# Kernel optimization log

Measured on AMD Instinct MI355X. Metric: run time of the kernel, lower is better.

## Reference

```python
import jax, jax.numpy as jnp
import numpy as np

S_DIM = 128            # attention head width s
E_DIM = 1024           # expansion e = 2*hidden
SQRT_S = 128.0 ** 0.5
EPS = 1e-5


def setup_inputs() -> dict:
    key = jax.random.key(0)
    ks = jax.random.split(key, 8)
    B, S, H = 64, 512, 512
    uv_dim = 2 * E_DIM + S_DIM  # 2176
    # xavier-uniform-ish scale for uv weight
    lim = (6.0 / (H + uv_dim)) ** 0.5
    return {
        "x": jax.random.normal(ks[0], (B, S, H), dtype=jnp.float32),
        "ln_g": jnp.ones((1,), dtype=jnp.float32),
        "uv_w": jax.random.uniform(ks[1], (uv_dim, H), minval=-lim, maxval=lim, dtype=jnp.float32),
        "uv_b": jnp.zeros((uv_dim,), dtype=jnp.float32),
        "gamma": jax.random.uniform(ks[2], (2, S_DIM), dtype=jnp.float32),
        "beta": jax.random.uniform(ks[3], (2, S_DIM), dtype=jnp.float32),
        "w_bias": jax.random.uniform(ks[4], (2 * S - 1,), dtype=jnp.float32),
        "o_w": jax.random.normal(ks[5], (H, E_DIM), dtype=jnp.float32) * 0.02,
        "o_b": jnp.zeros((H,), dtype=jnp.float32),
    }


def _rope(x):
    # x: [B, S, 2, s]; rotate along the sequence dim (dim=1)
    S = x.shape[1]
    half = x.shape[-1] // 2
    pos = jnp.arange(S, dtype=jnp.float32)
    # torch: freq_seq = -arange(half)/half; inv_freq = 10000**(-freq_seq)
    inv_freq = 10000.0 ** (jnp.arange(half, dtype=jnp.float32) / half)
    sinus = pos[:, None, None] * inv_freq[None, None, :]  # [S, 1, half]
    sin, cos = jnp.sin(sinus), jnp.cos(sinus)
    x1, x2 = x[..., :half], x[..., half:]
    return jnp.concatenate([x1 * cos - x2 * sin, x2 * cos + x1 * sin], axis=-1)


def reference(x, ln_g, uv_w, uv_b, gamma, beta, w_bias, o_w, o_b):
    B, S, H = x.shape
    # ScaleNorm
    norm = jnp.linalg.norm(x, axis=-1, keepdims=True) * (H ** -0.5)
    xn = x / jnp.maximum(norm, EPS) * ln_g
    # fused uv projection + SiLU
    act = jax.nn.silu(xn @ uv_w.T + uv_b)  # [B, S, 2e+s]
    u = act[..., :E_DIM]
    v = act[..., E_DIM:2 * E_DIM]
    base = act[..., 2 * E_DIM:]                      # [B, S, s]
    base = base[:, :, None, :] * gamma + beta        # [B, S, 2, s]
    base = _rope(base)
    q, k = base[:, :, 0, :], base[:, :, 1, :]
    # scores + relative position bias: bias[i, j] = w[j - i + S - 1]
    qk = jnp.einsum('bsd,btd->bst', q, k)
    idx = jnp.arange(S)[None, :] - jnp.arange(S)[:, None] + (S - 1)
    qk = qk + w_bias[idx]
    # relu2 similarity kernel
    kernel = jnp.square(jax.nn.relu(qk / SQRT_S))    # [B, S, S]
    out = u * jnp.einsum('bst,bte->bse', kernel, v)  # gated attention
    out = out @ o_w.T + o_b
    return out + x  # use_shortcut: hidden == output
```

## Files before the change

### kernel.cpp

```cpp
#include <hip/hip_runtime.h>
#include <math.h>


#define M_TOT   32768
#define S_LEN   512
#define H_DIM   512
#define E_DIMC  1024
#define UV_DIM  2176
#define UV_PAD  2304
#define D_DIM   128

using floatx4  = __attribute__((ext_vector_type(4))) float;
using uintx2   = __attribute__((ext_vector_type(2))) unsigned int;
using uintx4   = __attribute__((ext_vector_type(4))) unsigned int;
using ushortx4 = __attribute__((ext_vector_type(4))) unsigned short;
using short8   = __attribute__((ext_vector_type(8))) short;

#define ASYNC_CP16(gsrc, ldst)                                                  \
    __builtin_amdgcn_global_load_lds(                                           \
        (const __attribute__((address_space(1))) void*)(gsrc),                  \
        (__attribute__((address_space(3))) void*)(ldst), 16, 0, 0)

__device__ __forceinline__ float bf2f(unsigned short h) {
    union { unsigned int u; float f; } c;
    c.u = ((unsigned int)h) << 16;
    return c.f;
}
__device__ __forceinline__ unsigned short f2bf(float f) {
    union { float f; unsigned int u; } c;
    c.f = f;
    unsigned int r = c.u + 0x7fffu + ((c.u >> 16) & 1u);
    return (unsigned short)(r >> 16);
}
__device__ __forceinline__ float silu_fast(float x) {
    float e = __expf(-x);
    return x * __builtin_amdgcn_rcpf(1.0f + e);
}
__device__ __forceinline__ int xcd_remap(int b, int nwg) {
    return (b & 7) * (nwg >> 3) + (b >> 3);
}

__global__ __launch_bounds__(256) void f2bf_kernel(const float* __restrict__ in,
                                                   unsigned short* __restrict__ out,
                                                   int n4) {
    int i = blockIdx.x * 256 + threadIdx.x;
    if (i < n4) {
        floatx4 v = ((const floatx4*)in)[i];
        ushortx4 o;
        o.x = f2bf(v.x); o.y = f2bf(v.y); o.z = f2bf(v.z); o.w = f2bf(v.w);
        ((ushortx4*)out)[i] = o;
    }
}

__global__ __launch_bounds__(256) void f2bf_pad_kernel(const float* __restrict__ in,
                                                       unsigned short* __restrict__ out,
                                                       int n4_src, int n4_dst) {
    int i = blockIdx.x * 256 + threadIdx.x;
    if (i < n4_dst) {
        ushortx4 o;
        if (i < n4_src) {
            floatx4 v = ((const floatx4*)in)[i];
            o.x = f2bf(v.x); o.y = f2bf(v.y); o.z = f2bf(v.z); o.w = f2bf(v.w);
        } else {
            o.x = 0; o.y = 0; o.z = 0; o.w = 0;
        }
        ((ushortx4*)out)[i] = o;
    }
}

__global__ __launch_bounds__(256) void rmsnorm_kernel(const float* __restrict__ x,
                                                      const float* __restrict__ ln_g,
                                                      unsigned short* __restrict__ xn) {
    int row  = blockIdx.x * 4 + (threadIdx.x >> 6);
    int lane = threadIdx.x & 63;
    const float* xr = x + (size_t)row * H_DIM;
    floatx4 v0 = ((const floatx4*)xr)[lane];
    floatx4 v1 = ((const floatx4*)xr)[lane + 64];
    float ss = v0.x*v0.x + v0.y*v0.y + v0.z*v0.z + v0.w*v0.w
             + v1.x*v1.x + v1.y*v1.y + v1.z*v1.z + v1.w*v1.w;
    #pragma unroll
    for (int off = 32; off > 0; off >>= 1) ss += __shfl_xor(ss, off, 64);
    float norm = sqrtf(ss) * 0.044194173824159216f;
    float sc   = ln_g[0] / fmaxf(norm, 1e-5f);
    unsigned short* xo = xn + (size_t)row * H_DIM;
    ushortx4 o0, o1;
    o0.x = f2bf(v0.x * sc); o0.y = f2bf(v0.y * sc);
    o0.z = f2bf(v0.z * sc); o0.w = f2bf(v0.w * sc);
    o1.x = f2bf(v1.x * sc); o1.y = f2bf(v1.y * sc);
    o1.z = f2bf(v1.z * sc); o1.w = f2bf(v1.w * sc);
    ((ushortx4*)xo)[lane]      = o0;
    ((ushortx4*)xo)[lane + 64] = o1;
}

__global__ __launch_bounds__(64) void rope_table_kernel(float* __restrict__ cost,
                                                        float* __restrict__ sint) {
    int s = blockIdx.x;
    int j = threadIdx.x;
    float invf = (float)pow(10000.0, (double)j / 64.0);
    float ang  = (float)s * invf;
    double a   = (double)ang;
    cost[s * 64 + j] = (float)cos(a);
    sint[s * 64 + j] = (float)sin(a);
}

__global__ __launch_bounds__(256) void rope_apply_kernel(const float* __restrict__ base,
                                                         const float* __restrict__ gamma,
                                                         const float* __restrict__ beta,
                                                         const float* __restrict__ cost,
                                                         const float* __restrict__ sint,
                                                         unsigned short* __restrict__ q,
                                                         unsigned short* __restrict__ k) {
    int idx = blockIdx.x * 256 + threadIdx.x;
    int m = idx >> 6;
    int j = idx & 63;
    int s = m & (S_LEN - 1);
    float b1 = base[(size_t)m * D_DIM + j];
    float b2 = base[(size_t)m * D_DIM + 64 + j];
    float c  = cost[s * 64 + j];
    float sn = sint[s * 64 + j];
    float yq1 = b1 * gamma[j]       + beta[j];
    float yq2 = b2 * gamma[64 + j]  + beta[64 + j];
    float yk1 = b1 * gamma[128 + j] + beta[128 + j];
    float yk2 = b2 * gamma[192 + j] + beta[192 + j];
    q[(size_t)m * D_DIM + j]      = f2bf(yq1 * c - yq2 * sn);
    q[(size_t)m * D_DIM + 64 + j] = f2bf(yq2 * c + yq1 * sn);
    k[(size_t)m * D_DIM + j]      = f2bf(yk1 * c - yk2 * sn);
    k[(size_t)m * D_DIM + 64 + j] = f2bf(yk2 * c + yk1 * sn);
}

template <bool SWAPT>
__device__ __forceinline__ void gemm256_core(const unsigned short* __restrict__ A,
                                             const unsigned short* __restrict__ B,
                                             int lda, int ldb, int K,
                                             int m0, int n0,
                                             unsigned short (&st)[4][2][128][64],
                                             floatx4 (&acc)[8][4]) {
    const int tid  = threadIdx.x;
    const int lane = tid & 63;
    const int wave = tid >> 6;
    const int quad = lane >> 4;
    const int l16  = lane & 15;
    const int wrow = (wave >> 2) * 128;
    const int wcol = (wave & 3) * 64;

    const int q0    = wave * 128 + lane;
    const int R0    = q0 >> 3;
    const int cp0   = q0 & 7;
    const int c0    = cp0 ^ (R0 & 7);
    const int srow0 = 2 * R0 + (c0 >> 2);
    const int scol0 = (c0 & 3) * 8;

    const unsigned short* pa0 = A + (size_t)(m0 + srow0) * lda + scol0;
    const unsigned short* pa1 = pa0 + (size_t)16 * lda;
    const unsigned short* pb0 = B + (size_t)(n0 + srow0) * ldb + scol0;
    const unsigned short* pb1 = pb0 + (size_t)16 * ldb;
    const int ldsOff0 = (wave * 128) * 8;
    const int ldsOff1 = (wave * 128 + 64) * 8;

    #pragma unroll
    for (int i = 0; i < 8; i++)
        #pragma unroll
        for (int j = 0; j < 4; j++) acc[i][j] = (floatx4){0.f, 0.f, 0.f, 0.f};

    const int NT = K >> 5;
    auto stage = [&](int t) {
        unsigned short* sA = &st[t & 3][0][0][0];
        unsigned short* sB = &st[t & 3][1][0][0];
        const int kt = t * 32;
        ASYNC_CP16(pa0 + kt, sA + ldsOff0);
        ASYNC_CP16(pa1 + kt, sA + ldsOff1);
        ASYNC_CP16(pb0 + kt, sB + ldsOff0);
        ASYNC_CP16(pb1 + kt, sB + ldsOff1);
    };
    stage(0);
    stage(1);
    stage(2);

    int aoff[8], boff[4];
    #pragma unroll
    for (int mt = 0; mt < 8; mt++) {
        int r  = wrow + mt * 16 + l16;
        int Rr = r >> 1;
        int cp = (((r & 1) << 2) + quad) ^ (Rr & 7);
        aoff[mt] = Rr * 64 + cp * 8;
    }
    #pragma unroll
    for (int nt = 0; nt < 4; nt++) {
        int r  = wcol + nt * 16 + l16;
        int Rr = r >> 1;
        int cp = (((r & 1) << 2) + quad) ^ (Rr & 7);
        boff[nt] = Rr * 64 + cp * 8;
    }

    for (int t = 0; t < NT; ++t) {
        if (t < NT - 2)       asm volatile("s_waitcnt vmcnt(8)" ::: "memory");
        else if (t == NT - 2) asm volatile("s_waitcnt vmcnt(4)" ::: "memory");
        else                  asm volatile("s_waitcnt vmcnt(0)" ::: "memory");
        __builtin_amdgcn_sched_barrier(0);
        __builtin_amdgcn_s_barrier();
        __builtin_amdgcn_sched_barrier(0);
        if (t + 3 < NT) stage(t + 3);

        const unsigned short* sA = &st[t & 3][0][0][0];
        const unsigned short* sB = &st[t & 3][1][0][0];
        short8 bf[4];
        #pragma unroll
        for (int nt = 0; nt < 4; nt++) {
            union { short8 s8; uintx4 u4; } fu;
            fu.u4 = *(const uintx4*)&sB[boff[nt]];
            bf[nt] = fu.s8;
        }
        #pragma unroll
        for (int half = 0; half < 2; half++) {
            short8 af[4];
            #pragma unroll
            for (int mt = 0; mt < 4; mt++) {
                union { short8 s8; uintx4 u4; } fu;
                fu.u4 = *(const uintx4*)&sA[aoff[half * 4 + mt]];
                af[mt] = fu.s8;
            }
            __builtin_amdgcn_s_setprio(1);
            #pragma unroll
            for (int mt = 0; mt < 4; mt++)
                #pragma unroll
                for (int nt = 0; nt < 4; nt++)
                    acc[half * 4 + mt][nt] = SWAPT
                        ? __builtin_amdgcn_mfma_f32_16x16x32_bf16(bf[nt], af[mt], acc[half * 4 + mt][nt], 0, 0, 0)
                        : __builtin_amdgcn_mfma_f32_16x16x32_bf16(af[mt], bf[nt], acc[half * 4 + mt][nt], 0, 0, 0);
            __builtin_amdgcn_s_setprio(0);
        }
    }
}

union __align__(16) Lds256 {
    unsigned short st[4][2][128][64];
    unsigned short T[256 * 256];
};

__global__ __launch_bounds__(512, 2) void gemm1_256_kernel(const unsigned short* __restrict__ xn,
                                                           const unsigned short* __restrict__ uvw,
                                                           const float* __restrict__ uvb,
                                                           unsigned short* __restrict__ u,
                                                           unsigned short* __restrict__ vT,
                                                           float* __restrict__ base) {
    __shared__ Lds256 lds;
    floatx4 acc[8][4];
    const int bl = blockIdx.y * 9 + blockIdx.x;
    const int lg = xcd_remap(bl, 9 * (M_TOT / 256));
    const int xb = lg % 9;
    const int m0 = (lg / 9) * 256;
    const int tid = threadIdx.x, lane = tid & 63, wave = tid >> 6;
    const int quad = lane >> 4, l16 = lane & 15;
    const int wrow = (wave >> 2) * 128, wcol = (wave & 3) * 64;

    if (xb < 4) {
        const int n0 = xb * 256;
        gemm256_core<true>(xn, uvw, H_DIM, H_DIM, H_DIM, m0, n0, lds.st, acc);
        __syncthreads();
        #pragma unroll
        for (int mt = 0; mt < 8; mt++) {
            int row = wrow + mt * 16 + l16;
            #pragma unroll
            for (int nt = 0; nt < 4; nt++) {
                int nl = wcol + nt * 16 + quad * 4;
                floatx4 b4 = *(const floatx4*)&uvb[n0 + nl];
                ushortx4 pk;
                #pragma unroll
                for (int r = 0; r < 4; r++)
                    pk[r] = f2bf(silu_fast(acc[mt][nt][r] + b4[r]));
                *(uintx2*)&lds.T[row * 256 + (((nl >> 3) ^ (row & 15)) & 31) * 8 + (nl & 7)] = *(uintx2*)&pk;
            }
        }
        __syncthreads();
        #pragma unroll
        for (int i = 0; i < 16; i++) {
            int idx = tid + i * 512;
            int row = idx >> 5, c16 = idx & 31;
            *(uintx4*)(u + (size_t)(m0 + row) * E_DIMC + n0 + c16 * 8) =
                *(const uintx4*)&lds.T[row * 256 + ((c16 ^ (row & 15)) * 8)];
        }
    } else if (xb < 8) {
        const int n0 = xb * 256;
        gemm256_core<false>(xn, uvw, H_DIM, H_DIM, H_DIM, m0, n0, lds.st, acc);
        __syncthreads();
        #pragma unroll
        for (int nt = 0; nt < 4; nt++) {
            int rowT = wcol + nt * 16 + l16;
            float bias = uvb[n0 + rowT];
            #pragma unroll
            for (int mt = 0; mt < 8; mt++) {
                int colT = wrow + mt * 16 + quad * 4;
                ushortx4 pk;
                #pragma unroll
                for (int r = 0; r < 4; r++)
                    pk[r] = f2bf(silu_fast(acc[mt][nt][r] + bias));
                *(uintx2*)&lds.T[rowT * 256 + (((colT >> 3) ^ (rowT & 15)) & 31) * 8 + (colT & 7)] = *(uintx2*)&pk;
            }
        }
        __syncthreads();
        const int b = m0 >> 9, sg0 = m0 & (S_LEN - 1), eg0 = n0 - E_DIMC;
        #pragma unroll
        for (int i = 0; i < 16; i++) {
            int idx = tid + i * 512;
            int e = idx >> 5, c16 = idx & 31;
            *(uintx4*)(vT + ((size_t)b * E_DIMC + eg0 + e) * S_LEN + sg0 + c16 * 8) =
                *(const uintx4*)&lds.T[e * 256 + ((c16 ^ (e & 15)) * 8)];
        }
    } else {
        const int n0 = 2048;
        gemm256_core<false>(xn, uvw, H_DIM, H_DIM, H_DIM, m0, n0, lds.st, acc);
        if ((wave & 3) < 2) {
            #pragma unroll
            for (int mt = 0; mt < 8; mt++) {
                int m = m0 + wrow + mt * 16 + quad * 4;
                #pragma unroll
                for (int nt = 0; nt < 4; nt++) {
                    int n = wcol + nt * 16 + l16;
                    float bias = uvb[2048 + n];
                    #pragma unroll
                    for (int r = 0; r < 4; r++)
                        base[(size_t)(m + r) * D_DIM + n] = silu_fast(acc[mt][nt][r] + bias);
                }
            }
        }
    }
}

__global__ __launch_bounds__(512, 2) void gemm_out256_kernel(const unsigned short* __restrict__ oe,
                                                             const unsigned short* __restrict__ ow,
                                                             const float* __restrict__ ob,
                                                             const float* __restrict__ x,
                                                             float* __restrict__ out) {
    __shared__ __align__(16) unsigned short st[4][2][128][64];
    floatx4 acc[8][4];
    const int bl = blockIdx.y * 2 + blockIdx.x;
    const int lg = xcd_remap(bl, 2 * (M_TOT / 256));
    const int n0 = (lg & 1) * 256;
    const int m0 = (lg >> 1) * 256;
    gemm256_core<true>(oe, ow, E_DIMC, E_DIMC, E_DIMC, m0, n0, st, acc);

    const int tid = threadIdx.x, lane = tid & 63, wave = tid >> 6;
    const int quad = lane >> 4, l16 = lane & 15;
    const int wrow = (wave >> 2) * 128, wcol = (wave & 3) * 64;
    #pragma unroll
    for (int mt = 0; mt < 8; mt++) {
        int m = m0 + wrow + mt * 16 + l16;
        #pragma unroll
        for (int nt = 0; nt < 4; nt++) {
            int n = n0 + wcol + nt * 16 + quad * 4;
            size_t off = (size_t)m * H_DIM + n;
            floatx4 b4 = *(const floatx4*)&ob[n];
            floatx4 x4 = *(const floatx4*)&x[off];
            *(floatx4*)&out[off] = acc[mt][nt] + b4 + x4;
        }
    }
}

struct GemmLds {
    unsigned short As[128 * 64];
    unsigned short Bs[128 * 64];
};

template <bool SWAPT>
__device__ __forceinline__ void gemm_bt_core(const unsigned short* __restrict__ A,
                                             const unsigned short* __restrict__ B,
                                             int lda, int ldb, int K,
                                             int m0, int n0,
                                             GemmLds& lds, floatx4 (&acc)[4][4]) {
    const int tid  = threadIdx.x;
    const int lane = tid & 63;
    const int wave = tid >> 6;
    const int quad = lane >> 4;
    const int l16  = lane & 15;
    const int wm   = (wave >> 1) * 64;
    const int wn   = (wave & 1) * 64;
    const int lrow = lane >> 3;
    const int cgs  = ((lane & 7) ^ lrow) * 8;

    #pragma unroll
    for (int i = 0; i < 4; i++)
        #pragma unroll
        for (int j = 0; j < 4; j++) acc[i][j] = (floatx4){0.f, 0.f, 0.f, 0.f};

    for (int kt = 0; kt < K; kt += 64) {
        #pragma unroll
        for (int i = 0; i < 4; i++) {
            int r0 = wave * 32 + i * 8;
            const unsigned short* ga = A + (size_t)(m0 + r0 + lrow) * lda + kt + cgs;
            const unsigned short* gb = B + (size_t)(n0 + r0 + lrow) * ldb + kt + cgs;
            ASYNC_CP16(ga, &lds.As[r0 * 64]);
            ASYNC_CP16(gb, &lds.Bs[r0 * 64]);
        }
        __syncthreads();
        #pragma unroll
        for (int kk = 0; kk < 64; kk += 32) {
            short8 af[4], bf[4];
            const int pc = (kk + quad * 8) ^ ((l16 & 7) * 8);
            #pragma unroll
            for (int mt = 0; mt < 4; mt++) {
                int row = wm + mt * 16 + l16;
                union { short8 s8; uintx4 u4; } fu;
                fu.u4 = *(const uintx4*)&lds.As[row * 64 + pc];
                af[mt] = fu.s8;
            }
            #pragma unroll
            for (int nt = 0; nt < 4; nt++) {
                int row = wn + nt * 16 + l16;
                union { short8 s8; uintx4 u4; } fu;
                fu.u4 = *(const uintx4*)&lds.Bs[row * 64 + pc];
                bf[nt] = fu.s8;
            }
            #pragma unroll
            for (int mt = 0; mt < 4; mt++)
                #pragma unroll
                for (int nt = 0; nt < 4; nt++)
                    acc[mt][nt] = SWAPT
                        ? __builtin_amdgcn_mfma_f32_16x16x32_bf16(bf[nt], af[mt], acc[mt][nt], 0, 0, 0)
                        : __builtin_amdgcn_mfma_f32_16x16x32_bf16(af[mt], bf[nt], acc[mt][nt], 0, 0, 0);
        }
        __syncthreads();
    }
}

union LdsU {
    GemmLds g;
    unsigned short T[128 * 128];
};
__device__ __forceinline__ int swz(int row, int col) {
    return row * 128 + ((((col >> 3) ^ (row & 7)) << 3) | (col & 7));
}

__global__ __launch_bounds__(256) void gemm_qk_kernel(const unsigned short* __restrict__ q,
                                                      const unsigned short* __restrict__ k,
                                                      const float* __restrict__ wbias,
                                                      unsigned short* __restrict__ P) {
    __shared__ LdsU lds;
    floatx4 acc[4][4];
    const int bl = (blockIdx.z * 4 + blockIdx.y) * 4 + blockIdx.x;
    const int lg = xcd_remap(bl, 1024);
    const int bx = lg & 3, by = (lg >> 2) & 3, bz = lg >> 4;
    size_t boff = (size_t)bz * S_LEN * D_DIM;
    unsigned short* Pb = P + (size_t)bz * S_LEN * S_LEN;
    const int m0 = bx * 128, n0 = by * 128;
    gemm_bt_core<true>(q + boff, k + boff, D_DIM, D_DIM, D_DIM, m0, n0, lds.g, acc);

    const int tid = threadIdx.x, lane = tid & 63, wave = tid >> 6;
    const int quad = lane >> 4, l16 = lane & 15;
    const int wm = (wave >> 1) * 64, wn = (wave & 1) * 64;
    #pragma unroll
    for (int mt = 0; mt < 4; mt++) {
        int row = wm + mt * 16 + l16;
        int s   = m0 + row;
        #pragma unroll
        for (int nt = 0; nt < 4; nt++) {
            int nl = wn + nt * 16 + quad * 4;
            int t0 = n0 + nl;
            ushortx4 pk;
            #pragma unroll
            for (int r = 0; r < 4; r++) {
                float z = (acc[mt][nt][r] + wbias[t0 + r - s + (S_LEN - 1)]) * 0.08838834764831845f;
                z = fmaxf(z, 0.f);
                pk[r] = f2bf(z * z);
            }
            *(uintx2*)&lds.T[swz(row, nl)] = *(uintx2*)&pk;
        }
    }
    __syncthreads();
    #pragma unroll
    for (int i = 0; i < 8; i++) {
        int idx = tid + i * 256;
        int row = idx >> 4;
        int j   = idx & 15;
        *(uintx4*)(Pb + (size_t)(m0 + row) * S_LEN + n0 + j * 8) =
            *(const uintx4*)&lds.T[swz(row, j * 8)];
    }
}

__global__ __launch_bounds__(256) void gemm_pv_kernel(const unsigned short* __restrict__ P,
                                                      const unsigned short* __restrict__ vT,
                                                      unsigned short* __restrict__ u) {
    __shared__ LdsU lds;
    floatx4 acc[4][4];
    const int bl = (blockIdx.z * 8 + blockIdx.y) * 4 + blockIdx.x;
    const int lg = xcd_remap(bl, 2048);
    const int bx = lg & 3, by = (lg >> 2) & 7, bb = lg >> 5;
    const unsigned short* Pb  = P  + (size_t)bb * S_LEN * S_LEN;
    const unsigned short* vTb = vT + (size_t)bb * E_DIMC * S_LEN;
    const int m0 = bx * 128, n0 = by * 128;
    gemm_bt_core<true>(Pb, vTb, S_LEN, S_LEN, S_LEN, m0, n0, lds.g, acc);

    const int tid = threadIdx.x, lane = tid & 63, wave = tid >> 6;
    const int quad = lane >> 4, l16 = lane & 15;
    const int wm = (wave >> 1) * 64, wn = (wave & 1) * 64;
    #pragma unroll
    for (int mt = 0; mt < 4; mt++) {
        int row = wm + mt * 16 + l16;
        #pragma unroll
        for (int nt = 0; nt < 4; nt++) {
            int nl = wn + nt * 16 + quad * 4;
            ushortx4 pk;
            #pragma unroll
            for (int r = 0; r < 4; r++) pk[r] = f2bf(acc[mt][nt][r]);
            *(uintx2*)&lds.T[swz(row, nl)] = *(uintx2*)&pk;
        }
    }
    __syncthreads();
    #pragma unroll
    for (int i = 0; i < 8; i++) {
        int idx = tid + i * 256;
        int row = idx >> 4;
        int j   = idx & 15;
        size_t off = ((size_t)bb * S_LEN + m0 + row) * E_DIMC + n0 + j * 8;
        union { uintx4 u4; unsigned short s[8]; } tv, uv, ov;
        tv.u4 = *(const uintx4*)&lds.T[swz(row, j * 8)];
        uv.u4 = *(const uintx4*)(u + off);
        #pragma unroll
        for (int jj = 0; jj < 8; jj++) ov.s[jj] = f2bf(bf2f(tv.s[jj]) * bf2f(uv.s[jj]));
        *(uintx4*)(u + off) = ov.u4;
    }
}

extern "C" void kernel_launch(void* const* d_in, const int* in_sizes, int n_in,
                              void* d_out, int out_size, void* d_ws, size_t ws_size,
                              hipStream_t stream) {
    const float* x     = (const float*)d_in[0];
    const float* ln_g  = (const float*)d_in[1];
    const float* uv_w  = (const float*)d_in[2];
    const float* uv_b  = (const float*)d_in[3];
    const float* gamma = (const float*)d_in[4];
    const float* beta  = (const float*)d_in[5];
    const float* wbias = (const float*)d_in[6];
    const float* o_w   = (const float*)d_in[7];
    const float* o_b   = (const float*)d_in[8];
    float* out = (float*)d_out;

    char* ws = (char*)d_ws;
    size_t off = 0;
    auto alloc = [&](size_t bytes) {
        void* p = ws + off;
        off += (bytes + 255) & ~(size_t)255;
        return p;
    };
    unsigned short* u     = (unsigned short*)alloc((size_t)M_TOT * E_DIMC * 2);
    unsigned short* vT    = (unsigned short*)alloc((size_t)64 * E_DIMC * S_LEN * 2);
    unsigned short* xn    = (unsigned short*)alloc((size_t)M_TOT * H_DIM * 2);
    unsigned short* P     = xn;
    float*          base  = (float*)alloc((size_t)M_TOT * D_DIM * 4);
    unsigned short* q     = (unsigned short*)alloc((size_t)M_TOT * D_DIM * 2);
    unsigned short* k     = (unsigned short*)alloc((size_t)M_TOT * D_DIM * 2);
    float*          cost  = (float*)alloc((size_t)S_LEN * 64 * 4);
    float*          sint  = (float*)alloc((size_t)S_LEN * 64 * 4);
    unsigned short* uvwb  = (unsigned short*)alloc((size_t)UV_PAD * H_DIM * 2);
    unsigned short* owb   = (unsigned short*)alloc((size_t)H_DIM * E_DIMC * 2);
    (void)ws_size; (void)in_sizes; (void)n_in; (void)out_size;

    f2bf_pad_kernel<<<(UV_PAD * H_DIM / 4 + 255) / 256, 256, 0, stream>>>(
        uv_w, uvwb, UV_DIM * H_DIM / 4, UV_PAD * H_DIM / 4);
    f2bf_kernel<<<(H_DIM * E_DIMC / 4 + 255) / 256, 256, 0, stream>>>(o_w, owb, H_DIM * E_DIMC / 4);
    rope_table_kernel<<<S_LEN, 64, 0, stream>>>(cost, sint);

    rmsnorm_kernel<<<M_TOT / 4, 256, 0, stream>>>(x, ln_g, xn);

    gemm1_256_kernel<<<dim3(9, M_TOT / 256), 512, 0, stream>>>(xn, uvwb, uv_b, u, vT, base);

    rope_apply_kernel<<<M_TOT * 64 / 256, 256, 0, stream>>>(base, gamma, beta, cost, sint, q, k);

    gemm_qk_kernel<<<dim3(S_LEN / 128, S_LEN / 128, 64), 256, 0, stream>>>(q, k, wbias, P);

    gemm_pv_kernel<<<dim3(S_LEN / 128, E_DIMC / 128, 64), 256, 0, stream>>>(P, vT, u);

    gemm_out256_kernel<<<dim3(H_DIM / 256, M_TOT / 256), 512, 0, stream>>>(u, owb, o_b, x, out);
}
```

Measured before the change: 368.7 us.

## Shrink GEMM tiles to 128x256 with triple-buffered LDS and port PV to shared core

Replaces the 256x256 GEMM core (4-stage LDS ring) with a 128x256 core using a 3-buffer ring and smaller per-wave accumulators. The core is applied to the uv projection, the output projection, and a new 512-thread PV kernel that replaces the old 128x128 one. The intent is to lower LDS and register footprint per block so more blocks are resident, and to improve wave balance across CUs. In exchange each block gets less operand reuse and there is less prefetch depth.

```diff
diff --git a/kernel.cpp b/kernel.cpp
--- a/kernel.cpp
+++ b/kernel.cpp
@@ -129,56 +129,51 @@
 }
 
 template <bool SWAPT>
-__device__ __forceinline__ void gemm256_core(const unsigned short* __restrict__ A,
+__device__ __forceinline__ void gemm128_core(const unsigned short* __restrict__ A,
                                              const unsigned short* __restrict__ B,
                                              int lda, int ldb, int K,
                                              int m0, int n0,
-                                             unsigned short (&st)[4][2][128][64],
-                                             floatx4 (&acc)[8][4]) {
+                                             unsigned short (&st)[3][12288],
+                                             floatx4 (&acc)[4][4]) {
     const int tid  = threadIdx.x;
     const int lane = tid & 63;
     const int wave = tid >> 6;
     const int quad = lane >> 4;
     const int l16  = lane & 15;
-    const int wrow = (wave >> 2) * 128;
+    const int wrow = (wave >> 2) * 64;
     const int wcol = (wave & 3) * 64;
 
-    const int q0    = wave * 128 + lane;
-    const int R0    = q0 >> 3;
-    const int cp0   = q0 & 7;
-    const int c0    = cp0 ^ (R0 & 7);
-    const int srow0 = 2 * R0 + (c0 >> 2);
-    const int scol0 = (c0 & 3) * 8;
-
-    const unsigned short* pa0 = A + (size_t)(m0 + srow0) * lda + scol0;
-    const unsigned short* pa1 = pa0 + (size_t)16 * lda;
-    const unsigned short* pb0 = B + (size_t)(n0 + srow0) * ldb + scol0;
-    const unsigned short* pb1 = pb0 + (size_t)16 * ldb;
-    const int ldsOff0 = (wave * 128) * 8;
-    const int ldsOff1 = (wave * 128 + 64) * 8;
-
-    #pragma unroll
-    for (int i = 0; i < 8; i++)
+    const int qa  = wave * 64 + lane;
+    const int Ra  = qa >> 3;
+    const int ca  = (qa & 7) ^ (Ra & 7);
+    const int srA = 2 * Ra + (ca >> 2);
+    const int scA = (ca & 3) * 8;
+    const unsigned short* pa  = A + (size_t)(m0 + srA) * lda + scA;
+    const unsigned short* pb0 = B + (size_t)(n0 + srA) * ldb + scA;
+    const unsigned short* pb1 = pb0 + (size_t)128 * ldb;
+    const int ldsA  = (wave * 64) * 8;
+    const int ldsB0 = 4096 + (wave * 64) * 8;
+    const int ldsB1 = 4096 + (512 + wave * 64) * 8;
+
+    #pragma unroll
+    for (int i = 0; i < 4; i++)
         #pragma unroll
         for (int j = 0; j < 4; j++) acc[i][j] = (floatx4){0.f, 0.f, 0.f, 0.f};
 
     const int NT = K >> 5;
-    auto stage = [&](int t) {
-        unsigned short* sA = &st[t & 3][0][0][0];
-        unsigned short* sB = &st[t & 3][1][0][0];
+    auto stage = [&](int buf, int t) {
+        unsigned short* s = &st[buf][0];
         const int kt = t * 32;
-        ASYNC_CP16(pa0 + kt, sA + ldsOff0);
-        ASYNC_CP16(pa1 + kt, sA + ldsOff1);
-        ASYNC_CP16(pb0 + kt, sB + ldsOff0);
-        ASYNC_CP16(pb1 + kt, sB + ldsOff1);
+        ASYNC_CP16(pa  + kt, s + ldsA);
+        ASYNC_CP16(pb0 + kt, s + ldsB0);
+        ASYNC_CP16(pb1 + kt, s + ldsB1);
     };
-    stage(0);
-    stage(1);
-    stage(2);
-
-    int aoff[8], boff[4];
-    #pragma unroll
-    for (int mt = 0; mt < 8; mt++) {
+    stage(0, 0);
+    stage(1, 1);
+
+    int aoff[4], boff[4];
+    #pragma unroll
+    for (int mt = 0; mt < 4; mt++) {
         int r  = wrow + mt * 16 + l16;
         int Rr = r >> 1;
         int cp = (((r & 1) << 2) + quad) ^ (Rr & 7);
@@ -189,76 +184,74 @@
         int r  = wcol + nt * 16 + l16;
         int Rr = r >> 1;
         int cp = (((r & 1) << 2) + quad) ^ (Rr & 7);
-        boff[nt] = Rr * 64 + cp * 8;
-    }
-
+        boff[nt] = 4096 + Rr * 64 + cp * 8;
+    }
+
+    int bc = 0, bs = 2;
     for (int t = 0; t < NT; ++t) {
-        if (t < NT - 2)       asm volatile("s_waitcnt vmcnt(8)" ::: "memory");
-        else if (t == NT - 2) asm volatile("s_waitcnt vmcnt(4)" ::: "memory");
-        else                  asm volatile("s_waitcnt vmcnt(0)" ::: "memory");
+        if (t < NT - 1) asm volatile("s_waitcnt vmcnt(3)" ::: "memory");
+        else            asm volatile("s_waitcnt vmcnt(0)" ::: "memory");
         __builtin_amdgcn_sched_barrier(0);
         __builtin_amdgcn_s_barrier();
         __builtin_amdgcn_sched_barrier(0);
-        if (t + 3 < NT) stage(t + 3);
-
-        const unsigned short* sA = &st[t & 3][0][0][0];
-        const unsigned short* sB = &st[t & 3][1][0][0];
-        short8 bf[4];
+        if (t + 2 < NT) stage(bs, t + 2);
+
+        const unsigned short* sb = &st[bc][0];
+        short8 af[4], bf[4];
+        #pragma unroll
+        for (int mt = 0; mt < 4; mt++) {
+            union { short8 s8; uintx4 u4; } fu;
+            fu.u4 = *(const uintx4*)&sb[aoff[mt]];
+            af[mt] = fu.s8;
+        }
         #pragma unroll
         for (int nt = 0; nt < 4; nt++) {
             union { short8 s8; uintx4 u4; } fu;
-            fu.u4 = *(const uintx4*)&sB[boff[nt]];
+            fu.u4 = *(const uintx4*)&sb[boff[nt]];
             bf[nt] = fu.s8;
         }
-        #pragma unroll
-        for (int half = 0; half < 2; half++) {
-            short8 af[4];
-            #pragma unroll
-            for (int mt = 0; mt < 4; mt++) {
-                union { short8 s8; uintx4 u4; } fu;
-                fu.u4 = *(const uintx4*)&sA[aoff[half * 4 + mt]];
-                af[mt] = fu.s8;
-            }
-            __builtin_amdgcn_s_setprio(1);
-            #pragma unroll
-            for (int mt = 0; mt < 4; mt++)
-                #pragma unroll
-                for (int nt = 0; nt < 4; nt++)
-                    acc[half * 4 + mt][nt] = SWAPT
-                        ? __builtin_amdgcn_mfma_f32_16x16x32_bf16(bf[nt], af[mt], acc[half * 4 + mt][nt], 0, 0, 0)
-                        : __builtin_amdgcn_mfma_f32_16x16x32_bf16(af[mt], bf[nt], acc[half * 4 + mt][nt], 0, 0, 0);
-            __builtin_amdgcn_s_setprio(0);
-        }
-    }
-}
-
-union __align__(16) Lds256 {
-    unsigned short st[4][2][128][64];
-    unsigned short T[256 * 256];
+        __builtin_amdgcn_s_setprio(1);
+        #pragma unroll
+        for (int mt = 0; mt < 4; mt++)
+            #pragma unroll
+            for (int nt = 0; nt < 4; nt++)
+                acc[mt][nt] = SWAPT
+                    ? __builtin_amdgcn_mfma_f32_16x16x32_bf16(bf[nt], af[mt], acc[mt][nt], 0, 0, 0)
+                    : __builtin_amdgcn_mfma_f32_16x16x32_bf16(af[mt], bf[nt], acc[mt][nt], 0, 0, 0);
+        __builtin_amdgcn_s_setprio(0);
+
+        bc = (bc == 2) ? 0 : bc + 1;
+        bs = (bs == 2) ? 0 : bs + 1;
+    }
+}
+
+union __align__(16) Lds3 {
+    unsigned short st[3][12288];
+    unsigned short T[128 * 256];
 };
 
-__global__ __launch_bounds__(512, 2) void gemm1_256_kernel(const unsigned short* __restrict__ xn,
+__global__ __launch_bounds__(512, 2) void gemm1_128_kernel(const unsigned short* __restrict__ xn,
                                                            const unsigned short* __restrict__ uvw,
                                                            const float* __restrict__ uvb,
                                                            unsigned short* __restrict__ u,
                                                            unsigned short* __restrict__ vT,
                                                            float* __restrict__ base) {
-    __shared__ Lds256 lds;
-    floatx4 acc[8][4];
+    __shared__ Lds3 lds;
+    floatx4 acc[4][4];
     const int bl = blockIdx.y * 9 + blockIdx.x;
-    const int lg = xcd_remap(bl, 9 * (M_TOT / 256));
+    const int lg = xcd_remap(bl, 9 * (M_TOT / 128));
     const int xb = lg % 9;
-    const int m0 = (lg / 9) * 256;
+    const int m0 = (lg / 9) * 128;
     const int tid = threadIdx.x, lane = tid & 63, wave = tid >> 6;
     const int quad = lane >> 4, l16 = lane & 15;
-    const int wrow = (wave >> 2) * 128, wcol = (wave & 3) * 64;
+    const int wrow = (wave >> 2) * 64, wcol = (wave & 3) * 64;
 
     if (xb < 4) {
         const int n0 = xb * 256;
-        gemm256_core<true>(xn, uvw, H_DIM, H_DIM, H_DIM, m0, n0, lds.st, acc);
+        gemm128_core<true>(xn, uvw, H_DIM, H_DIM, H_DIM, m0, n0, lds.st, acc);
         __syncthreads();
         #pragma unroll
-        for (int mt = 0; mt < 8; mt++) {
+        for (int mt = 0; mt < 4; mt++) {
             int row = wrow + mt * 16 + l16;
             #pragma unroll
             for (int nt = 0; nt < 4; nt++) {
@@ -268,50 +261,50 @@
                 #pragma unroll
                 for (int r = 0; r < 4; r++)
                     pk[r] = f2bf(silu_fast(acc[mt][nt][r] + b4[r]));
-                *(uintx2*)&lds.T[row * 256 + (((nl >> 3) ^ (row & 15)) & 31) * 8 + (nl & 7)] = *(uintx2*)&pk;
+                *(uintx2*)&lds.T[row * 256 + (((nl >> 3) ^ (row & 15)) << 3) + (nl & 7)] = *(uintx2*)&pk;
             }
         }
         __syncthreads();
         #pragma unroll
-        for (int i = 0; i < 16; i++) {
+        for (int i = 0; i < 8; i++) {
             int idx = tid + i * 512;
             int row = idx >> 5, c16 = idx & 31;
             *(uintx4*)(u + (size_t)(m0 + row) * E_DIMC + n0 + c16 * 8) =
-                *(const uintx4*)&lds.T[row * 256 + ((c16 ^ (row & 15)) * 8)];
+                *(const uintx4*)&lds.T[row * 256 + ((c16 ^ (row & 15)) << 3)];
         }
     } else if (xb < 8) {
         const int n0 = xb * 256;
-        gemm256_core<false>(xn, uvw, H_DIM, H_DIM, H_DIM, m0, n0, lds.st, acc);
+        gemm128_core<false>(xn, uvw, H_DIM, H_DIM, H_DIM, m0, n0, lds.st, acc);
         __syncthreads();
         #pragma unroll
         for (int nt = 0; nt < 4; nt++) {
             int rowT = wcol + nt * 16 + l16;
             float bias = uvb[n0 + rowT];
             #pragma unroll
-            for (int mt = 0; mt < 8; mt++) {
+            for (int mt = 0; mt < 4; mt++) {
                 int colT = wrow + mt * 16 + quad * 4;
                 ushortx4 pk;
                 #pragma unroll
                 for (int r = 0; r < 4; r++)
                     pk[r] = f2bf(silu_fast(acc[mt][nt][r] + bias));
-                *(uintx2*)&lds.T[rowT * 256 + (((colT >> 3) ^ (rowT & 15)) & 31) * 8 + (colT & 7)] = *(uintx2*)&pk;
+                *(uintx2*)&lds.T[rowT * 128 + (((colT >> 3) ^ (rowT & 15)) << 3) + (colT & 7)] = *(uintx2*)&pk;
             }
         }
         __syncthreads();
         const int b = m0 >> 9, sg0 = m0 & (S_LEN - 1), eg0 = n0 - E_DIMC;
         #pragma unroll
-        for (int i = 0; i < 16; i++) {
+        for (int i = 0; i < 8; i++) {
             int idx = tid + i * 512;
-            int e = idx >> 5, c16 = idx & 31;
-            *(uintx4*)(vT + ((size_t)b * E_DIMC + eg0 + e) * S_LEN + sg0 + c16 * 8) =
-                *(const uintx4*)&lds.T[e * 256 + ((c16 ^ (e & 15)) * 8)];
+            int e = idx >> 4, j = idx & 15;
+            *(uintx4*)(vT + ((size_t)b * E_DIMC + eg0 + e) * S_LEN + sg0 + j * 8) =
+                *(const uintx4*)&lds.T[e * 128 + ((j ^ (e & 15)) << 3)];
         }
     } else {
         const int n0 = 2048;
-        gemm256_core<false>(xn, uvw, H_DIM, H_DIM, H_DIM, m0, n0, lds.st, acc);
+        gemm128_core<false>(xn, uvw, H_DIM, H_DIM, H_DIM, m0, n0, lds.st, acc);
         if ((wave & 3) < 2) {
             #pragma unroll
-            for (int mt = 0; mt < 8; mt++) {
+            for (int mt = 0; mt < 4; mt++) {
                 int m = m0 + wrow + mt * 16 + quad * 4;
                 #pragma unroll
                 for (int nt = 0; nt < 4; nt++) {
@@ -326,24 +319,24 @@
     }
 }
 
-__global__ __launch_bounds__(512, 2) void gemm_out256_kernel(const unsigned short* __restrict__ oe,
+__global__ __launch_bounds__(512, 2) void gemm_out128_kernel(const unsigned short* __restrict__ oe,
                                                              const unsigned short* __restrict__ ow,
                                                              const float* __restrict__ ob,
                                                              const float* __restrict__ x,
                                                              float* __restrict__ out) {
-    __shared__ __align__(16) unsigned short st[4][2][128][64];
-    floatx4 acc[8][4];
+    __shared__ __align__(16) unsigned short st[3][12288];
+    floatx4 acc[4][4];
     const int bl = blockIdx.y * 2 + blockIdx.x;
-    const int lg = xcd_remap(bl, 2 * (M_TOT / 256));
+    const int lg = xcd_remap(bl, 2 * (M_TOT / 128));
     const int n0 = (lg & 1) * 256;
-    const int m0 = (lg >> 1) * 256;
-    gemm256_core<true>(oe, ow, E_DIMC, E_DIMC, E_DIMC, m0, n0, st, acc);
+    const int m0 = (lg >> 1) * 128;
+    gemm128_core<true>(oe, ow, E_DIMC, E_DIMC, E_DIMC, m0, n0, st, acc);
 
     const int tid = threadIdx.x, lane = tid & 63, wave = tid >> 6;
     const int quad = lane >> 4, l16 = lane & 15;
-    const int wrow = (wave >> 2) * 128, wcol = (wave & 3) * 64;
-    #pragma unroll
-    for (int mt = 0; mt < 8; mt++) {
+    const int wrow = (wave >> 2) * 64, wcol = (wave & 3) * 64;
+    #pragma unroll
+    for (int mt = 0; mt < 4; mt++) {
         int m = m0 + wrow + mt * 16 + l16;
         #pragma unroll
         for (int nt = 0; nt < 4; nt++) {
@@ -353,6 +346,50 @@
             floatx4 x4 = *(const floatx4*)&x[off];
             *(floatx4*)&out[off] = acc[mt][nt] + b4 + x4;
         }
+    }
+}
+
+__global__ __launch_bounds__(512, 2) void gemm_pv128_kernel(const unsigned short* __restrict__ P,
+                                                            const unsigned short* __restrict__ vT,
+                                                            unsigned short* __restrict__ u) {
+    __shared__ Lds3 lds;
+    floatx4 acc[4][4];
+    const int bl = (blockIdx.z * 4 + blockIdx.y) * 4 + blockIdx.x;
+    const int lg = xcd_remap(bl, 1024);
+    const int bx = lg & 3, by = (lg >> 2) & 3, bb = lg >> 4;
+    const unsigned short* Pb  = P  + (size_t)bb * S_LEN * S_LEN;
+    const unsigned short* vTb = vT + (size_t)bb * E_DIMC * S_LEN;
+    const int m0 = bx * 128, n0 = by * 256;
+    gemm128_core<true>(Pb, vTb, S_LEN, S_LEN, S_LEN, m0, n0, lds.st, acc);
+
+    const int tid = threadIdx.x, lane = tid & 63, wave = tid >> 6;
+    const int quad = lane >> 4, l16 = lane & 15;
+    const int wrow = (wave >> 2) * 64, wcol = (wave & 3) * 64;
+    __syncthreads();
+    #pragma unroll
+    for (int mt = 0; mt < 4; mt++) {
+        int row = wrow + mt * 16 + l16;
+        #pragma unroll
+        for (int nt = 0; nt < 4; nt++) {
+            int nl = wcol + nt * 16 + quad * 4;
+            ushortx4 pk;
+            #pragma unroll
+            for (int r = 0; r < 4; r++) pk[r] = f2bf(acc[mt][nt][r]);
+            *(uintx2*)&lds.T[row * 256 + (((nl >> 3) ^ (row & 15)) << 3) + (nl & 7)] = *(uintx2*)&pk;
+        }
+    }
+    __syncthreads();
+    #pragma unroll
+    for (int i = 0; i < 8; i++) {
+        int idx = tid + i * 512;
+        int row = idx >> 5, c16 = idx & 31;
+        size_t off = ((size_t)bb * S_LEN + m0 + row) * E_DIMC + n0 + c16 * 8;
+        union { uintx4 u4; unsigned short s[8]; } tv, uv, ov;
+        tv.u4 = *(const uintx4*)&lds.T[row * 256 + ((c16 ^ (row & 15)) << 3)];
+        uv.u4 = *(const uintx4*)(u + off);
+        #pragma unroll
+        for (int jj = 0; jj < 8; jj++) ov.s[jj] = f2bf(bf2f(tv.s[jj]) * bf2f(uv.s[jj]));
+        *(uintx4*)(u + off) = ov.u4;
     }
 }
 
@@ -473,50 +510,6 @@
         int j   = idx & 15;
         *(uintx4*)(Pb + (size_t)(m0 + row) * S_LEN + n0 + j * 8) =
             *(const uintx4*)&lds.T[swz(row, j * 8)];
-    }
-}
-
-__global__ __launch_bounds__(256) void gemm_pv_kernel(const unsigned short* __restrict__ P,
-                                                      const unsigned short* __restrict__ vT,
-                                                      unsigned short* __restrict__ u) {
-    __shared__ LdsU lds;
-    floatx4 acc[4][4];
-    const int bl = (blockIdx.z * 8 + blockIdx.y) * 4 + blockIdx.x;
-    const int lg = xcd_remap(bl, 2048);
-    const int bx = lg & 3, by = (lg >> 2) & 7, bb = lg >> 5;
-    const unsigned short* Pb  = P  + (size_t)bb * S_LEN * S_LEN;
-    const unsigned short* vTb = vT + (size_t)bb * E_DIMC * S_LEN;
-    const int m0 = bx * 128, n0 = by * 128;
-    gemm_bt_core<true>(Pb, vTb, S_LEN, S_LEN, S_LEN, m0, n0, lds.g, acc);
-
-    const int tid = threadIdx.x, lane = tid & 63, wave = tid >> 6;
-    const int quad = lane >> 4, l16 = lane & 15;
-    const int wm = (wave >> 1) * 64, wn = (wave & 1) * 64;
-    #pragma unroll
-    for (int mt = 0; mt < 4; mt++) {
-        int row = wm + mt * 16 + l16;
-        #pragma unroll
-        for (int nt = 0; nt < 4; nt++) {
-            int nl = wn + nt * 16 + quad * 4;
-            ushortx4 pk;
-            #pragma unroll
-            for (int r = 0; r < 4; r++) pk[r] = f2bf(acc[mt][nt][r]);
-            *(uintx2*)&lds.T[swz(row, nl)] = *(uintx2*)&pk;
-        }
-    }
-    __syncthreads();
-    #pragma unroll
-    for (int i = 0; i < 8; i++) {
-        int idx = tid + i * 256;
-        int row = idx >> 4;
-        int j   = idx & 15;
-        size_t off = ((size_t)bb * S_LEN + m0 + row) * E_DIMC + n0 + j * 8;
-        union { uintx4 u4; unsigned short s[8]; } tv, uv, ov;
-        tv.u4 = *(const uintx4*)&lds.T[swz(row, j * 8)];
-        uv.u4 = *(const uintx4*)(u + off);
-        #pragma unroll
-        for (int jj = 0; jj < 8; jj++) ov.s[jj] = f2bf(bf2f(tv.s[jj]) * bf2f(uv.s[jj]));
-        *(uintx4*)(u + off) = ov.u4;
     }
 }
 
@@ -561,13 +554,13 @@
 
     rmsnorm_kernel<<<M_TOT / 4, 256, 0, stream>>>(x, ln_g, xn);
 
-    gemm1_256_kernel<<<dim3(9, M_TOT / 256), 512, 0, stream>>>(xn, uvwb, uv_b, u, vT, base);
+    gemm1_128_kernel<<<dim3(9, M_TOT / 128), 512, 0, stream>>>(xn, uvwb, uv_b, u, vT, base);
 
     rope_apply_kernel<<<M_TOT * 64 / 256, 256, 0, stream>>>(base, gamma, beta, cost, sint, q, k);
 
     gemm_qk_kernel<<<dim3(S_LEN / 128, S_LEN / 128, 64), 256, 0, stream>>>(q, k, wbias, P);
 
-    gemm_pv_kernel<<<dim3(S_LEN / 128, E_DIMC / 128, 64), 256, 0, stream>>>(P, vT, u);
-
-    gemm_out256_kernel<<<dim3(H_DIM / 256, M_TOT / 256), 512, 0, stream>>>(u, owb, o_b, x, out);
-}
+    gemm_pv128_kernel<<<dim3(S_LEN / 128, E_DIMC / 256, 64), 512, 0, stream>>>(P, vT, u);
+
+    gemm_out128_kernel<<<dim3(H_DIM / 256, M_TOT / 128), 512, 0, stream>>>(u, owb, o_b, x, out);
+}
```

Result: no change. 365.8 us (-0.8%).

## Replace 256x256 uv-projection GEMM with 128x256 tiles and triple-buffered pipeline

Applied to the files above, without the earlier changes.

The fused uv projection GEMM now uses 128-row by 256-column tiles instead of 256x256, doubling the number of blocks. The new core streams K in 32-wide steps through a three-stage async LDS ring with a single barrier per step, which shrinks LDS and register use so more blocks can be resident. The intent is better occupancy, less tail imbalance and more latency hiding. In exchange each tile reuses data less, so more operand traffic goes through L2, and there are more barriers per unit of work.

```diff
diff --git a/kernel.cpp b/kernel.cpp
--- a/kernel.cpp
+++ b/kernel.cpp
@@ -129,6 +129,197 @@
 }
 
 template <bool SWAPT>
+__device__ __forceinline__ void gemm128_core(const unsigned short* __restrict__ A,
+                                             const unsigned short* __restrict__ B,
+                                             int lda, int ldb, int K,
+                                             int m0, int n0,
+                                             unsigned short (&st)[3][12288],
+                                             floatx4 (&acc)[4][4]) {
+    const int tid  = threadIdx.x;
+    const int lane = tid & 63;
+    const int wave = tid >> 6;
+    const int quad = lane >> 4;
+    const int l16  = lane & 15;
+    const int wrow = (wave >> 2) * 64;
+    const int wcol = (wave & 3) * 64;
+
+    const int qa  = wave * 64 + lane;
+    const int Ra  = qa >> 3;
+    const int ca  = (qa & 7) ^ (Ra & 7);
+    const int srA = 2 * Ra + (ca >> 2);
+    const int scA = (ca & 3) * 8;
+    const unsigned short* pa  = A + (size_t)(m0 + srA) * lda + scA;
+    const unsigned short* pb0 = B + (size_t)(n0 + srA) * ldb + scA;
+    const unsigned short* pb1 = pb0 + (size_t)128 * ldb;
+    const int ldsA  = (wave * 64) * 8;
+    const int ldsB0 = 4096 + (wave * 64) * 8;
+    const int ldsB1 = 4096 + (512 + wave * 64) * 8;
+
+    #pragma unroll
+    for (int i = 0; i < 4; i++)
+        #pragma unroll
+        for (int j = 0; j < 4; j++) acc[i][j] = (floatx4){0.f, 0.f, 0.f, 0.f};
+
+    const int NT = K >> 5;
+    auto stage = [&](int buf, int t) {
+        unsigned short* s = &st[buf][0];
+        const int kt = t * 32;
+        ASYNC_CP16(pa  + kt, s + ldsA);
+        ASYNC_CP16(pb0 + kt, s + ldsB0);
+        ASYNC_CP16(pb1 + kt, s + ldsB1);
+    };
+    stage(0, 0);
+    stage(1, 1);
+
+    int aoff[4], boff[4];
+    #pragma unroll
+    for (int mt = 0; mt < 4; mt++) {
+        int r  = wrow + mt * 16 + l16;
+        int Rr = r >> 1;
+        int cp = (((r & 1) << 2) + quad) ^ (Rr & 7);
+        aoff[mt] = Rr * 64 + cp * 8;
+    }
+    #pragma unroll
+    for (int nt = 0; nt < 4; nt++) {
+        int r  = wcol + nt * 16 + l16;
+        int Rr = r >> 1;
+        int cp = (((r & 1) << 2) + quad) ^ (Rr & 7);
+        boff[nt] = 4096 + Rr * 64 + cp * 8;
+    }
+
+    int bc = 0, bs = 2;
+    for (int t = 0; t < NT; ++t) {
+        if (t < NT - 1) asm volatile("s_waitcnt vmcnt(3)" ::: "memory");
+        else            asm volatile("s_waitcnt vmcnt(0)" ::: "memory");
+        __builtin_amdgcn_sched_barrier(0);
+        __builtin_amdgcn_s_barrier();
+        __builtin_amdgcn_sched_barrier(0);
+        if (t + 2 < NT) stage(bs, t + 2);
+
+        const unsigned short* sb = &st[bc][0];
+        short8 af[4], bf[4];
+        #pragma unroll
+        for (int mt = 0; mt < 4; mt++) {
+            union { short8 s8; uintx4 u4; } fu;
+            fu.u4 = *(const uintx4*)&sb[aoff[mt]];
+            af[mt] = fu.s8;
+        }
+        #pragma unroll
+        for (int nt = 0; nt < 4; nt++) {
+            union { short8 s8; uintx4 u4; } fu;
+            fu.u4 = *(const uintx4*)&sb[boff[nt]];
+            bf[nt] = fu.s8;
+        }
+        __builtin_amdgcn_s_setprio(1);
+        #pragma unroll
+        for (int mt = 0; mt < 4; mt++)
+            #pragma unroll
+            for (int nt = 0; nt < 4; nt++)
+                acc[mt][nt] = SWAPT
+                    ? __builtin_amdgcn_mfma_f32_16x16x32_bf16(bf[nt], af[mt], acc[mt][nt], 0, 0, 0)
+                    : __builtin_amdgcn_mfma_f32_16x16x32_bf16(af[mt], bf[nt], acc[mt][nt], 0, 0, 0);
+        __builtin_amdgcn_s_setprio(0);
+
+        bc = (bc == 2) ? 0 : bc + 1;
+        bs = (bs == 2) ? 0 : bs + 1;
+    }
+}
+
+union __align__(16) Lds3 {
+    unsigned short st[3][12288];
+    unsigned short T[128 * 256];
+};
+
+__global__ __launch_bounds__(512, 2) void gemm1_128_kernel(const unsigned short* __restrict__ xn,
+                                                           const unsigned short* __restrict__ uvw,
+                                                           const float* __restrict__ uvb,
+                                                           unsigned short* __restrict__ u,
+                                                           unsigned short* __restrict__ vT,
+                                                           float* __restrict__ base) {
+    __shared__ Lds3 lds;
+    floatx4 acc[4][4];
+    const int bl = blockIdx.y * 9 + blockIdx.x;
+    const int lg = xcd_remap(bl, 9 * (M_TOT / 128));
+    const int xb = lg % 9;
+    const int m0 = (lg / 9) * 128;
+    const int tid = threadIdx.x, lane = tid & 63, wave = tid >> 6;
+    const int quad = lane >> 4, l16 = lane & 15;
+    const int wrow = (wave >> 2) * 64, wcol = (wave & 3) * 64;
+
+    if (xb < 4) {
+        const int n0 = xb * 256;
+        gemm128_core<true>(xn, uvw, H_DIM, H_DIM, H_DIM, m0, n0, lds.st, acc);
+        __syncthreads();
+        #pragma unroll
+        for (int mt = 0; mt < 4; mt++) {
+            int row = wrow + mt * 16 + l16;
+            #pragma unroll
+            for (int nt = 0; nt < 4; nt++) {
+                int nl = wcol + nt * 16 + quad * 4;
+                floatx4 b4 = *(const floatx4*)&uvb[n0 + nl];
+                ushortx4 pk;
+                #pragma unroll
+                for (int r = 0; r < 4; r++)
+                    pk[r] = f2bf(silu_fast(acc[mt][nt][r] + b4[r]));
+                *(uintx2*)&lds.T[row * 256 + (((nl >> 3) ^ (row & 15)) << 3) + (nl & 7)] = *(uintx2*)&pk;
+            }
+        }
+        __syncthreads();
+        #pragma unroll
+        for (int i = 0; i < 8; i++) {
+            int idx = tid + i * 512;
+            int row = idx >> 5, c16 = idx & 31;
+            *(uintx4*)(u + (size_t)(m0 + row) * E_DIMC + n0 + c16 * 8) =
+                *(const uintx4*)&lds.T[row * 256 + ((c16 ^ (row & 15)) << 3)];
+        }
+    } else if (xb < 8) {
+        const int n0 = xb * 256;
+        gemm128_core<false>(xn, uvw, H_DIM, H_DIM, H_DIM, m0, n0, lds.st, acc);
+        __syncthreads();
+        #pragma unroll
+        for (int nt = 0; nt < 4; nt++) {
+            int rowT = wcol + nt * 16 + l16;
+            float bias = uvb[n0 + rowT];
+            #pragma unroll
+            for (int mt = 0; mt < 4; mt++) {
+                int colT = wrow + mt * 16 + quad * 4;
+                ushortx4 pk;
+                #pragma unroll
+                for (int r = 0; r < 4; r++)
+                    pk[r] = f2bf(silu_fast(acc[mt][nt][r] + bias));
+                *(uintx2*)&lds.T[rowT * 128 + (((colT >> 3) ^ (rowT & 15)) << 3) + (colT & 7)] = *(uintx2*)&pk;
+            }
+        }
+        __syncthreads();
+        const int b = m0 >> 9, sg0 = m0 & (S_LEN - 1), eg0 = n0 - E_DIMC;
+        #pragma unroll
+        for (int i = 0; i < 8; i++) {
+            int idx = tid + i * 512;
+            int e = idx >> 4, j = idx & 15;
+            *(uintx4*)(vT + ((size_t)b * E_DIMC + eg0 + e) * S_LEN + sg0 + j * 8) =
+                *(const uintx4*)&lds.T[e * 128 + ((j ^ (e & 15)) << 3)];
+        }
+    } else {
+        const int n0 = 2048;
+        gemm128_core<false>(xn, uvw, H_DIM, H_DIM, H_DIM, m0, n0, lds.st, acc);
+        if ((wave & 3) < 2) {
+            #pragma unroll
+            for (int mt = 0; mt < 4; mt++) {
+                int m = m0 + wrow + mt * 16 + quad * 4;
+                #pragma unroll
+                for (int nt = 0; nt < 4; nt++) {
+                    int n = wcol + nt * 16 + l16;
+                    float bias = uvb[2048 + n];
+                    #pragma unroll
+                    for (int r = 0; r < 4; r++)
+                        base[(size_t)(m + r) * D_DIM + n] = silu_fast(acc[mt][nt][r] + bias);
+                }
+            }
+        }
+    }
+}
+
+template <bool SWAPT>
 __device__ __forceinline__ void gemm256_core(const unsigned short* __restrict__ A,
                                              const unsigned short* __restrict__ B,
                                              int lda, int ldb, int K,
@@ -228,100 +419,6 @@
                         ? __builtin_amdgcn_mfma_f32_16x16x32_bf16(bf[nt], af[mt], acc[half * 4 + mt][nt], 0, 0, 0)
                         : __builtin_amdgcn_mfma_f32_16x16x32_bf16(af[mt], bf[nt], acc[half * 4 + mt][nt], 0, 0, 0);
             __builtin_amdgcn_s_setprio(0);
-        }
-    }
-}
-
-union __align__(16) Lds256 {
-    unsigned short st[4][2][128][64];
-    unsigned short T[256 * 256];
-};
-
-__global__ __launch_bounds__(512, 2) void gemm1_256_kernel(const unsigned short* __restrict__ xn,
-                                                           const unsigned short* __restrict__ uvw,
-                                                           const float* __restrict__ uvb,
-                                                           unsigned short* __restrict__ u,
-                                                           unsigned short* __restrict__ vT,
-                                                           float* __restrict__ base) {
-    __shared__ Lds256 lds;
-    floatx4 acc[8][4];
-    const int bl = blockIdx.y * 9 + blockIdx.x;
-    const int lg = xcd_remap(bl, 9 * (M_TOT / 256));
-    const int xb = lg % 9;
-    const int m0 = (lg / 9) * 256;
-    const int tid = threadIdx.x, lane = tid & 63, wave = tid >> 6;
-    const int quad = lane >> 4, l16 = lane & 15;
-    const int wrow = (wave >> 2) * 128, wcol = (wave & 3) * 64;
-
-    if (xb < 4) {
-        const int n0 = xb * 256;
-        gemm256_core<true>(xn, uvw, H_DIM, H_DIM, H_DIM, m0, n0, lds.st, acc);
-        __syncthreads();
-        #pragma unroll
-        for (int mt = 0; mt < 8; mt++) {
-            int row = wrow + mt * 16 + l16;
-            #pragma unroll
-            for (int nt = 0; nt < 4; nt++) {
-                int nl = wcol + nt * 16 + quad * 4;
-                floatx4 b4 = *(const floatx4*)&uvb[n0 + nl];
-                ushortx4 pk;
-                #pragma unroll
-                for (int r = 0; r < 4; r++)
-                    pk[r] = f2bf(silu_fast(acc[mt][nt][r] + b4[r]));
-                *(uintx2*)&lds.T[row * 256 + (((nl >> 3) ^ (row & 15)) & 31) * 8 + (nl & 7)] = *(uintx2*)&pk;
-            }
-        }
-        __syncthreads();
-        #pragma unroll
-        for (int i = 0; i < 16; i++) {
-            int idx = tid + i * 512;
-            int row = idx >> 5, c16 = idx & 31;
-            *(uintx4*)(u + (size_t)(m0 + row) * E_DIMC + n0 + c16 * 8) =
-                *(const uintx4*)&lds.T[row * 256 + ((c16 ^ (row & 15)) * 8)];
-        }
-    } else if (xb < 8) {
-        const int n0 = xb * 256;
-        gemm256_core<false>(xn, uvw, H_DIM, H_DIM, H_DIM, m0, n0, lds.st, acc);
-        __syncthreads();
-        #pragma unroll
-        for (int nt = 0; nt < 4; nt++) {
-            int rowT = wcol + nt * 16 + l16;
-            float bias = uvb[n0 + rowT];
-            #pragma unroll
-            for (int mt = 0; mt < 8; mt++) {
-                int colT = wrow + mt * 16 + quad * 4;
-                ushortx4 pk;
-                #pragma unroll
-                for (int r = 0; r < 4; r++)
-                    pk[r] = f2bf(silu_fast(acc[mt][nt][r] + bias));
-                *(uintx2*)&lds.T[rowT * 256 + (((colT >> 3) ^ (rowT & 15)) & 31) * 8 + (colT & 7)] = *(uintx2*)&pk;
-            }
-        }
-        __syncthreads();
-        const int b = m0 >> 9, sg0 = m0 & (S_LEN - 1), eg0 = n0 - E_DIMC;
-        #pragma unroll
-        for (int i = 0; i < 16; i++) {
-            int idx = tid + i * 512;
-            int e = idx >> 5, c16 = idx & 31;
-            *(uintx4*)(vT + ((size_t)b * E_DIMC + eg0 + e) * S_LEN + sg0 + c16 * 8) =
-                *(const uintx4*)&lds.T[e * 256 + ((c16 ^ (e & 15)) * 8)];
-        }
-    } else {
-        const int n0 = 2048;
-        gemm256_core<false>(xn, uvw, H_DIM, H_DIM, H_DIM, m0, n0, lds.st, acc);
-        if ((wave & 3) < 2) {
-            #pragma unroll
-            for (int mt = 0; mt < 8; mt++) {
-                int m = m0 + wrow + mt * 16 + quad * 4;
-                #pragma unroll
-                for (int nt = 0; nt < 4; nt++) {
-                    int n = wcol + nt * 16 + l16;
-                    float bias = uvb[2048 + n];
-                    #pragma unroll
-                    for (int r = 0; r < 4; r++)
-                        base[(size_t)(m + r) * D_DIM + n] = silu_fast(acc[mt][nt][r] + bias);
-                }
-            }
         }
     }
 }
@@ -561,7 +658,7 @@
 
     rmsnorm_kernel<<<M_TOT / 4, 256, 0, stream>>>(x, ln_g, xn);
 
-    gemm1_256_kernel<<<dim3(9, M_TOT / 256), 512, 0, stream>>>(xn, uvwb, uv_b, u, vT, base);
+    gemm1_128_kernel<<<dim3(9, M_TOT / 128), 512, 0, stream>>>(xn, uvwb, uv_b, u, vT, base);
 
     rope_apply_kernel<<<M_TOT * 64 / 256, 256, 0, stream>>>(base, gamma, beta, cost, sint, q, k);
 
```

Measured after the change: 357.6 us. 3.0% less time.
